# Optimization experiments

Measured on AMD Instinct MI355X. Metric: run time of the kernel, lower is better.

Reference implementation:

```python
import jax, jax.numpy as jnp
import numpy as np

B, H, W, C = 16, 64, 64, 256
WIN, SHIFT, HEADS, NSTYLE, HID = 8, 4, 8, 512, 1024
HB = HEADS // 2   # heads per attention branch
CB = C // 2       # channels per branch
N = WIN * WIN     # tokens per window
EPS = 1e-5


def _rel_index(w):
    coords = np.stack(np.meshgrid(np.arange(w), np.arange(w), indexing='ij'))  # [2,w,w]
    cf = coords.reshape(2, -1)
    rel = (cf[:, :, None] - cf[:, None, :]).transpose(1, 2, 0)  # [N,N,2]
    rel[:, :, 0] += w - 1
    rel[:, :, 1] += w - 1
    rel[:, :, 0] *= 2 * w - 1
    return rel.sum(-1)  # [N,N]


def _sw_mask(Hh, Ww, w, shift):
    img = np.zeros((Hh, Ww))
    cnt = 0
    for hs in (slice(0, -w), slice(-w, -shift), slice(-shift, None)):
        for ws in (slice(0, -w), slice(-w, -shift), slice(-shift, None)):
            img[hs, ws] = cnt
            cnt += 1
    win = img.reshape(Hh // w, w, Ww // w, w).transpose(0, 2, 1, 3).reshape(-1, w * w)
    m = win[:, None, :] - win[:, :, None]
    return np.where(m != 0, -100.0, 0.0).astype(np.float32)  # [nW,N,N]


REL_IDX = _rel_index(WIN)
SW_MASK = jnp.asarray(_sw_mask(H, W, WIN, SHIFT))


def window_partition(x):
    # x: [B,H,W,c] -> [B*nW, N, c]
    b, hh, ww, c = x.shape
    x = x.reshape(b, hh // WIN, WIN, ww // WIN, WIN, c).transpose(0, 1, 3, 2, 4, 5)
    return x.reshape(-1, N, c)


def window_reverse(win):
    c = win.shape[-1]
    x = win.reshape(B, H // WIN, W // WIN, WIN, WIN, c).transpose(0, 1, 3, 2, 4, 5)
    return x.reshape(B, H, W, c)


def _adain(x, style, Wa, ba):
    # x: [B,L,C]; instance norm over L per channel, then style affine
    s = style @ Wa + ba                      # [B, 2C]
    mu_s, std_s = jnp.split(s, 2, axis=1)    # each [B,C]
    mu = x.mean(axis=1, keepdims=True)
    var = ((x - mu) ** 2).mean(axis=1, keepdims=True)
    xn = (x - mu) * jax.lax.rsqrt(var + EPS)
    return mu_s[:, None, :] + std_s[:, None, :] * xn


def _win_attn(q, k, v, rpb, mask):
    # q,k,v: [B_, N, CB]; rpb: [(2w-1)^2, HB]; mask: [nW,N,N] or None
    B_ = q.shape[0]
    d = CB // HB
    q = q.reshape(B_, N, HB, d).transpose(0, 2, 1, 3) * (d ** -0.5)
    k = k.reshape(B_, N, HB, d).transpose(0, 2, 1, 3)
    v = v.reshape(B_, N, HB, d).transpose(0, 2, 1, 3)
    attn = jnp.einsum('bhnd,bhmd->bhnm', q, k)
    bias = rpb[REL_IDX.reshape(-1)].reshape(N, N, HB).transpose(2, 0, 1)
    attn = attn + bias[None]
    if mask is not None:
        nW = mask.shape[0]
        attn = attn.reshape(B_ // nW, nW, HB, N, N) + mask[None, :, None]
        attn = attn.reshape(B_, HB, N, N)
    attn = jax.nn.softmax(attn, axis=-1)
    out = jnp.einsum('bhnm,bhmd->bhnd', attn, v)
    return out.transpose(0, 2, 1, 3).reshape(B_, N, CB)


def setup_inputs() -> dict:
    key = jax.random.key(0)
    ks = jax.random.split(key, 20)
    f = jnp.float32
    return {
        'x': jax.random.normal(ks[0], (B, H * W, C), f),
        'style': jax.random.normal(ks[1], (B, NSTYLE), f),
        'w_qkv': jax.random.normal(ks[2], (C, 3 * C), f) * 0.02,
        'b_qkv': jnp.zeros((3 * C,), f),
        'w_proj': jax.random.normal(ks[3], (C, C), f) * 0.02,
        'b_proj': jnp.zeros((C,), f),
        'w_ada1': jax.random.normal(ks[4], (NSTYLE, 2 * C), f) * 0.02,
        'b_ada1': jnp.concatenate([jnp.zeros((C,), f), jnp.ones((C,), f)]),
        'w_ada2': jax.random.normal(ks[5], (NSTYLE, 2 * C), f) * 0.02,
        'b_ada2': jnp.concatenate([jnp.zeros((C,), f), jnp.ones((C,), f)]),
        'rpb1': jax.random.normal(ks[6], ((2 * WIN - 1) ** 2, HB), f) * 0.02,
        'rpb2': jax.random.normal(ks[7], ((2 * WIN - 1) ** 2, HB), f) * 0.02,
        'w_fc1': jax.random.normal(ks[8], (C, HID), f) * 0.02,
        'b_fc1': jnp.zeros((HID,), f),
        'w_fc2': jax.random.normal(ks[9], (HID, C), f) * 0.02,
        'b_fc2': jnp.zeros((C,), f),
    }


def reference(x, style, w_qkv, b_qkv, w_proj, b_proj, w_ada1, b_ada1,
              w_ada2, b_ada2, rpb1, rpb2, w_fc1, b_fc1, w_fc2, b_fc2):
    Bn, L, Cc = x.shape
    # AdaIN 1
    h = _adain(x, style, w_ada1, b_ada1)                      # [B,L,C]
    qkv = (h @ w_qkv + b_qkv).reshape(Bn, H, W, 3, Cc)
    q, k, v = qkv[..., 0, :], qkv[..., 1, :], qkv[..., 2, :]  # [B,H,W,C]
    # split channels across the two branches
    q1, k1, v1 = q[..., :CB], k[..., :CB], v[..., :CB]
    q2, k2, v2 = q[..., CB:], k[..., CB:], v[..., CB:]
    shift = lambda t: jnp.roll(t, (-SHIFT, -SHIFT), axis=(1, 2))
    # W-MSA branch
    x_w = _win_attn(window_partition(q1), window_partition(k1),
                    window_partition(v1), rpb1, None)
    # SW-MSA branch (shifted windows + mask)
    x_sw = _win_attn(window_partition(shift(q2)), window_partition(shift(k2)),
                     window_partition(shift(v2)), rpb2, SW_MASK)
    xw = window_reverse(x_w)                                  # [B,H,W,CB]
    xsw = jnp.roll(window_reverse(x_sw), (SHIFT, SHIFT), axis=(1, 2))
    attn_out = jnp.concatenate([xw, xsw], axis=-1).reshape(Bn, L, Cc)
    x = x + attn_out @ w_proj + b_proj
    # AdaIN 2 + MLP (exact GELU, as nn.GELU default)
    h2 = _adain(x, style, w_ada2, b_ada2)
    h2 = jax.nn.gelu(h2 @ w_fc1 + b_fc1, approximate=False)
    return x + (h2 @ w_fc2 + b_fc2)
```

## Files before the change

### kernel.cpp

```cpp
#include <hip/hip_runtime.h>
#include <hip/hip_bf16.h>

typedef __bf16 bf16;
typedef __bf16 bf16x4v __attribute__((ext_vector_type(4)));
typedef __bf16 bf16x8v __attribute__((ext_vector_type(8)));
typedef float f32x4 __attribute__((ext_vector_type(4)));
typedef short s16x4 __attribute__((ext_vector_type(4)));

#define DEVINL static __device__ __forceinline__

DEVINL f32x4 mfma16(bf16x8v a, bf16x8v b, f32x4 c) {
  return __builtin_amdgcn_mfma_f32_16x16x32_bf16(a, b, c, 0, 0, 0);
}

DEVINL f32x4 mfma16x16(bf16x4v a, bf16x4v b, f32x4 c) {
#if __has_builtin(__builtin_amdgcn_mfma_f32_16x16x16bf16_1k)
  return __builtin_amdgcn_mfma_f32_16x16x16bf16_1k(
      __builtin_bit_cast(s16x4, a), __builtin_bit_cast(s16x4, b), c, 0, 0, 0);
#else
  f32x4 d;
  asm("v_mfma_f32_16x16x16_bf16 %0, %1, %2, %3"
      : "=v"(d) : "v"(a), "v"(b), "v"(c));
  return d;
#endif
}

__global__ __launch_bounds__(256) void k_style(
    const float* __restrict__ style,
    const float* __restrict__ wa1, const float* __restrict__ ba1,
    const float* __restrict__ wa2, const float* __restrict__ ba2,
    float* __restrict__ s1, float* __restrict__ s2) {
  int bid = blockIdx.x;
  int ng = bid & 31, b = (bid >> 5) & 15, which = bid >> 9;
  int tid = threadIdx.x;
  int nl = tid & 15, kg = tid >> 4;
  int n = ng * 16 + nl;
  const float* wa = which ? wa2 : wa1;
  const float* ba = which ? ba2 : ba1;
  const float* srow = style + b * 512;
  float acc = 0.f;
  #pragma unroll 8
  for (int kk = 0; kk < 32; ++kk) {
    int k = kg + kk * 16;
    acc += srow[k] * wa[k * 512 + n];
  }
  acc += __shfl_xor(acc, 16);
  acc += __shfl_xor(acc, 32);
  __shared__ float red[4][16];
  int l = tid & 63, w = tid >> 6;
  if (l < 16) red[w][nl] = acc;
  __syncthreads();
  if (tid < 16) {
    float S = red[0][tid] + red[1][tid] + red[2][tid] + red[3][tid]
            + ba[ng * 16 + tid];
    (which ? s2 : s1)[b * 512 + ng * 16 + tid] = S;
  }
}

template<int F32>
__global__ __launch_bounds__(256) void k_stats_part(
    const void* __restrict__ xv, float* __restrict__ psum,
    float* __restrict__ psq) {
  int rc = blockIdx.x, b = blockIdx.y;
  int c = threadIdx.x;
  size_t base = (size_t)b * 4096 * 256 + (size_t)rc * 256 * 256 + c;
  float sm = 0.f, q = 0.f;
  #pragma unroll 4
  for (int r = 0; r < 256; ++r) {
    float f;
    if constexpr (F32) f = ((const float*)xv)[base + (size_t)r * 256];
    else               f = (float)((const bf16*)xv)[base + (size_t)r * 256];
    sm += f; q += f * f;
  }
  int o = (b * 16 + rc) * 256 + c;
  psum[o] = sm; psq[o] = q;
}

__global__ __launch_bounds__(256) void k_stats_fin(
    const float* __restrict__ psum, const float* __restrict__ psq,
    const float* __restrict__ s,
    float* __restrict__ scale, float* __restrict__ shift) {
  int b = blockIdx.x, c = threadIdx.x;
  float S = 0.f, Q = 0.f;
  #pragma unroll
  for (int rc = 0; rc < 16; ++rc) {
    S += psum[(b * 16 + rc) * 256 + c];
    Q += psq[(b * 16 + rc) * 256 + c];
  }
  float mean = S * (1.0f/4096.0f);
  float var  = Q * (1.0f/4096.0f) - mean * mean;
  float inv  = rsqrtf(var + 1e-5f);
  float mu_s  = s[b * 512 + c];
  float std_s = s[b * 512 + 256 + c];
  float sc = std_s * inv;
  scale[b * 256 + c] = sc;
  shift[b * 256 + c] = mu_s - sc * mean;
}

template<int F32>
__global__ __launch_bounds__(256) void k_adain(
    const void* __restrict__ in, const float* __restrict__ scale,
    const float* __restrict__ shift, bf16* __restrict__ out) {
  int idx = blockIdx.x * 256 + threadIdx.x;
  int c8 = idx & 31, row = idx >> 5;
  int b = row >> 12, c = c8 * 8;
  const float* scp = &scale[b * 256 + c];
  const float* shp = &shift[b * 256 + c];
  f32x4 sc0 = *(const f32x4*)scp, sc1 = *(const f32x4*)(scp + 4);
  f32x4 sh0 = *(const f32x4*)shp, sh1 = *(const f32x4*)(shp + 4);
  size_t ofs = (size_t)row * 256 + c;
  float f[8];
  if constexpr (F32) {
    f32x4 v0 = *(const f32x4*)&((const float*)in)[ofs];
    f32x4 v1 = *(const f32x4*)&((const float*)in)[ofs + 4];
    f[0]=v0[0]; f[1]=v0[1]; f[2]=v0[2]; f[3]=v0[3];
    f[4]=v1[0]; f[5]=v1[1]; f[6]=v1[2]; f[7]=v1[3];
  } else {
    bf16x8v v = *(const bf16x8v*)&((const bf16*)in)[ofs];
    #pragma unroll
    for (int u = 0; u < 8; ++u) f[u] = (float)v[u];
  }
  bf16x8v o;
  o[0]=(bf16)(sh0[0]+sc0[0]*f[0]); o[1]=(bf16)(sh0[1]+sc0[1]*f[1]);
  o[2]=(bf16)(sh0[2]+sc0[2]*f[2]); o[3]=(bf16)(sh0[3]+sc0[3]*f[3]);
  o[4]=(bf16)(sh1[0]+sc1[0]*f[4]); o[5]=(bf16)(sh1[1]+sc1[1]*f[5]);
  o[6]=(bf16)(sh1[2]+sc1[2]*f[6]); o[7]=(bf16)(sh1[3]+sc1[3]*f[7]);
  *(bf16x8v*)&out[ofs] = o;
}

__global__ __launch_bounds__(256) void k_tr(
    const float* __restrict__ in, bf16* __restrict__ out, int K, int N) {
  __shared__ float t[32][33];
  int bx = blockIdx.x * 32, by = blockIdx.y * 32;
  int tx = threadIdx.x & 31, ty = threadIdx.x >> 5;
  #pragma unroll
  for (int r = 0; r < 32; r += 8)
    t[ty + r][tx] = in[(size_t)(by + ty + r) * N + bx + tx];
  __syncthreads();
  #pragma unroll
  for (int r = 0; r < 32; r += 8)
    out[(size_t)(bx + ty + r) * K + by + tx] = (bf16)t[tx][ty + r];
}

template<int RESMODE, int GELU, int OUTF32>
__global__ __launch_bounds__(512) void k_gemm(
    const bf16* __restrict__ A, const bf16* __restrict__ Bt,
    const float* __restrict__ bias, const void* __restrict__ resv,
    void* __restrict__ outv, int N, int K, int gx) {
  __shared__ bf16 a_sw[256 * 64];
  __shared__ bf16 b_sw[128 * 64];
  int tid = threadIdx.x;
  int l = tid & 63, w = tid >> 6;
  int wr = w >> 1, wc = w & 1;
  int lm = l & 15, lg = l >> 4;

  int nwg = gridDim.x;
  int lin = blockIdx.x;
  int swz = (lin & 7) * (nwg >> 3) + (lin >> 3);
  int bx = swz % gx, by = swz / gx;
  int m0 = by * 256, n0 = bx * 128;

  f32x4 acc[4][4];
  #pragma unroll
  for (int mi = 0; mi < 4; ++mi)
    #pragma unroll
    for (int ni = 0; ni < 4; ++ni)
      acc[mi][ni] = (f32x4){0.f, 0.f, 0.f, 0.f};

  for (int k0 = 0; k0 < K; k0 += 64) {
    #pragma unroll
    for (int i = 0; i < 4; ++i) {
      int slot = i * 512 + tid;
      int r = slot >> 3, cs = slot & 7;
      int c = cs ^ (r & 7);
      const bf16* g = A + (size_t)(m0 + r) * K + k0 + c * 8;
      __builtin_amdgcn_global_load_lds(
          (const __attribute__((address_space(1))) void*)g,
          (__attribute__((address_space(3))) void*)(a_sw + (i * 512 + w * 64) * 8),
          16, 0, 0);
    }
    #pragma unroll
    for (int i = 0; i < 2; ++i) {
      int slot = i * 512 + tid;
      int r = slot >> 3, cs = slot & 7;
      int c = cs ^ (r & 7);
      const bf16* g = Bt + (size_t)(n0 + r) * K + k0 + c * 8;
      __builtin_amdgcn_global_load_lds(
          (const __attribute__((address_space(1))) void*)g,
          (__attribute__((address_space(3))) void*)(b_sw + (i * 512 + w * 64) * 8),
          16, 0, 0);
    }
    __syncthreads();
    #pragma unroll
    for (int kk = 0; kk < 2; ++kk) {
      bf16x8v af[4], bv[4];
      #pragma unroll
      for (int mi = 0; mi < 4; ++mi) {
        int row = wr * 64 + mi * 16 + lm;
        af[mi] = *(const bf16x8v*)&a_sw[row * 64 + (((kk * 4 + lg) ^ (row & 7)) * 8)];
      }
      #pragma unroll
      for (int ni = 0; ni < 4; ++ni) {
        int row = wc * 64 + ni * 16 + lm;
        bv[ni] = *(const bf16x8v*)&b_sw[row * 64 + (((kk * 4 + lg) ^ (row & 7)) * 8)];
      }
      #pragma unroll
      for (int mi = 0; mi < 4; ++mi)
        #pragma unroll
        for (int ni = 0; ni < 4; ++ni)
          acc[mi][ni] = mfma16(af[mi], bv[ni], acc[mi][ni]);
    }
    __syncthreads();
  }
  #pragma unroll
  for (int mi = 0; mi < 4; ++mi) {
    #pragma unroll
    for (int ni = 0; ni < 4; ++ni) {
      int row = m0 + wr * 64 + mi * 16 + lg * 4;
      int col = n0 + wc * 64 + ni * 16 + lm;
      float bv_ = bias[col];
      #pragma unroll
      for (int j = 0; j < 4; ++j) {
        float o = acc[mi][ni][j] + bv_;
        if constexpr (RESMODE == 1)
          o += ((const float*)resv)[(size_t)(row + j) * N + col];
        if constexpr (RESMODE == 2)
          o += (float)((const bf16*)resv)[(size_t)(row + j) * N + col];
        if constexpr (GELU) {
          float z = 1.5957691216057308f * (o + 0.044715f * o * o * o);
          o = o / (1.0f + __expf(-z));
        }
        if constexpr (OUTF32)
          ((float*)outv)[(size_t)(row + j) * N + col] = o;
        else
          ((bf16*)outv)[(size_t)(row + j) * N + col] = (bf16)o;
      }
    }
  }
}

__global__ __launch_bounds__(256) void k_attn(
    const bf16* __restrict__ qkv,
    const float* __restrict__ rpb1, const float* __restrict__ rpb2,
    bf16* __restrict__ aout) {
  __shared__ bf16 vt[128 * 72];
  __shared__ float rl[960];

  int tid = threadIdx.x;
  int bx = blockIdx.x;
  int br = bx & 1, widx = (bx >> 1) & 63, b = bx >> 7;
  int wy = widx >> 3, wx = widx & 7;

  const float* rpb = br ? rpb2 : rpb1;
  #pragma unroll
  for (int t = tid; t < 960; t += 256) {
    int h0 = t / 240, r0 = t - h0 * 240, dy = r0 >> 4, dx = r0 & 15;
    rl[t] = (dx < 15) ? rpb[(dy * 15 + dx) * 4 + h0] : 0.f;
  }

  auto grow = [&](int tok) -> int {
    int y = wy * 8 + (tok >> 3), xc = wx * 8 + (tok & 7);
    if (br) { y = (y + 4) & 63; xc = (xc + 4) & 63; }
    return b * 4096 + y * 64 + xc;
  };

  #pragma unroll
  for (int it = 0; it < 4; ++it) {
    int task = it * 256 + tid;
    int tok = task & 63, chunk = task >> 6;
    bf16x8v v = *(const bf16x8v*)&qkv[(size_t)grow(tok) * 768 + 512 + br * 128 + chunk * 8];
    #pragma unroll
    for (int u = 0; u < 8; ++u) vt[(chunk * 8 + u) * 72 + tok] = v[u];
  }

  int l = tid & 63, h = tid >> 6;
  int lm = l & 15, lg = l >> 4;

  bf16x8v kb[4], qa[4];
  #pragma unroll
  for (int i = 0; i < 4; ++i) {
    size_t rb = (size_t)grow(i * 16 + lm) * 768 + br * 128 + h * 32 + lg * 8;
    qa[i] = *(const bf16x8v*)&qkv[rb];
    kb[i] = *(const bf16x8v*)&qkv[rb + 256];
  }
  __syncthreads();

  bf16x4v vb[2][4];
  #pragma unroll
  for (int ni = 0; ni < 2; ++ni)
    #pragma unroll
    for (int ki = 0; ki < 4; ++ki)
      vb[ni][ki] = *(const bf16x4v*)&vt[(h * 32 + ni * 16 + lm) * 72 + ki * 16 + lg * 4];

  bool need_mask = br && (wy == 7 || wx == 7);

  int ekA[16], idkA[16];
  #pragma unroll
  for (int ki = 0; ki < 4; ++ki)
    #pragma unroll
    for (int j = 0; j < 4; ++j) {
      int ik = ki * 16 + lg * 4 + j;
      ekA[ki * 4 + j] = ik + (ik >> 3) * 8;
      int yk = wy * 8 + (ik >> 3), xk = wx * 8 + (ik & 7);
      idkA[ki * 4 + j] = (yk < 56 ? 0 : (yk < 60 ? 1 : 2)) * 3
                       + (xk < 56 ? 0 : (xk < 60 ? 1 : 2));
    }

  #pragma unroll
  for (int qi = 0; qi < 4; ++qi) {
    f32x4 s[4];
    #pragma unroll
    for (int ki = 0; ki < 4; ++ki)
      s[ki] = mfma16(kb[ki], qa[qi], (f32x4){0.f,0.f,0.f,0.f});

    int iq = qi * 16 + lm;
    int eq = iq + (iq >> 3) * 8;
    int yq = wy * 8 + (iq >> 3), xq = wx * 8 + (iq & 7);
    int idq = (yq < 56 ? 0 : (yq < 60 ? 1 : 2)) * 3
            + (xq < 56 ? 0 : (xq < 60 ? 1 : 2));
    const float* fb = &rl[h * 240 + 119 + eq];

    #pragma unroll
    for (int ki = 0; ki < 4; ++ki)
      #pragma unroll
      for (int j = 0; j < 4; ++j) {
        float val = s[ki][j] * 0.17677669529663687f + fb[-ekA[ki * 4 + j]];
        if (need_mask && idq != idkA[ki * 4 + j]) val -= 100.0f;
        s[ki][j] = val;
      }

    float mx = s[0][0];
    #pragma unroll
    for (int ki = 0; ki < 4; ++ki)
      #pragma unroll
      for (int j = 0; j < 4; ++j) mx = fmaxf(mx, s[ki][j]);
    mx = fmaxf(mx, __shfl_xor(mx, 16));
    mx = fmaxf(mx, __shfl_xor(mx, 32));
    float sum = 0.f;
    #pragma unroll
    for (int ki = 0; ki < 4; ++ki)
      #pragma unroll
      for (int j = 0; j < 4; ++j) {
        float e = __expf(s[ki][j] - mx);
        s[ki][j] = e;
        sum += e;
      }
    sum += __shfl_xor(sum, 16);
    sum += __shfl_xor(sum, 32);
    float rs = 1.0f / sum;

    bf16x4v pa[4];
    #pragma unroll
    for (int ki = 0; ki < 4; ++ki)
      #pragma unroll
      for (int j = 0; j < 4; ++j)
        pa[ki][j] = (bf16)(s[ki][j] * rs);

    f32x4 o[2] = {(f32x4){0.f,0.f,0.f,0.f}, (f32x4){0.f,0.f,0.f,0.f}};
    #pragma unroll
    for (int ki = 0; ki < 4; ++ki) {
      o[0] = mfma16x16(pa[ki], vb[0][ki], o[0]);
      o[1] = mfma16x16(pa[ki], vb[1][ki], o[1]);
    }

    #pragma unroll
    for (int ni = 0; ni < 2; ++ni)
      #pragma unroll
      for (int j = 0; j < 4; ++j) {
        int tok = qi * 16 + lg * 4 + j;
        int col = br * 128 + h * 32 + ni * 16 + lm;
        aout[(size_t)grow(tok) * 256 + col] = (bf16)o[ni][j];
      }
  }
}

extern "C" void kernel_launch(void* const* d_in, const int* in_sizes, int n_in,
                              void* d_out, int out_size, void* d_ws, size_t ws_size,
                              hipStream_t stream) {
  (void)in_sizes; (void)n_in; (void)out_size; (void)ws_size;
  const float* x      = (const float*)d_in[0];
  const float* style  = (const float*)d_in[1];
  const float* w_qkv  = (const float*)d_in[2];
  const float* b_qkv  = (const float*)d_in[3];
  const float* w_proj = (const float*)d_in[4];
  const float* b_proj = (const float*)d_in[5];
  const float* w_ada1 = (const float*)d_in[6];
  const float* b_ada1 = (const float*)d_in[7];
  const float* w_ada2 = (const float*)d_in[8];
  const float* b_ada2 = (const float*)d_in[9];
  const float* rpb1   = (const float*)d_in[10];
  const float* rpb2   = (const float*)d_in[11];
  const float* w_fc1  = (const float*)d_in[12];
  const float* b_fc1  = (const float*)d_in[13];
  const float* w_fc2  = (const float*)d_in[14];
  const float* b_fc2  = (const float*)d_in[15];

  char* ws = (char*)d_ws;
  float* s1     = (float*)(ws + 0);
  float* s2     = (float*)(ws + 32768);
  float* scale1 = (float*)(ws + 65536);
  float* shift1 = (float*)(ws + 81920);
  float* scale2 = (float*)(ws + 98304);
  float* shift2 = (float*)(ws + 114688);
  bf16* wtqkv   = (bf16*)(ws + 131072);
  bf16* wtproj  = (bf16*)(ws + 524288);
  bf16* wtfc1   = (bf16*)(ws + 655360);
  bf16* wtfc2   = (bf16*)(ws + 1179648);
  float* psum   = (float*)(ws + 1703936);
  float* psq    = (float*)(ws + 1966080);
  const size_t BIG = 2228224;
  bf16* xn   = (bf16*)(ws + BIG);
  bf16* qkv  = (bf16*)(ws + BIG + 33554432);
  bf16* attn = (bf16*)(ws + BIG + 134217728);
  bf16* x1   = (bf16*)(ws + BIG + 33554432);
  bf16* xn2  = xn;
  bf16* g    = (bf16*)(ws + BIG + 67108864);

  k_tr<<<dim3(24, 8),  256, 0, stream>>>(w_qkv,  wtqkv,  256, 768);
  k_tr<<<dim3(8, 8),   256, 0, stream>>>(w_proj, wtproj, 256, 256);
  k_tr<<<dim3(32, 8),  256, 0, stream>>>(w_fc1,  wtfc1,  256, 1024);
  k_tr<<<dim3(8, 32),  256, 0, stream>>>(w_fc2,  wtfc2,  1024, 256);

  k_style<<<1024, 256, 0, stream>>>(style, w_ada1, b_ada1, w_ada2, b_ada2, s1, s2);
  k_stats_part<1><<<dim3(16, 16), 256, 0, stream>>>(x, psum, psq);
  k_stats_fin<<<16, 256, 0, stream>>>(psum, psq, s1, scale1, shift1);
  k_adain<1><<<8192, 256, 0, stream>>>(x, scale1, shift1, xn);

  k_gemm<0,0,0><<<1536, 512, 0, stream>>>(
      xn, wtqkv, b_qkv, nullptr, qkv, 768, 256, 6);

  k_attn<<<2048, 256, 0, stream>>>(qkv, rpb1, rpb2, attn);

  k_gemm<1,0,0><<<512, 512, 0, stream>>>(
      attn, wtproj, b_proj, x, x1, 256, 256, 2);

  k_stats_part<0><<<dim3(16, 16), 256, 0, stream>>>(x1, psum, psq);
  k_stats_fin<<<16, 256, 0, stream>>>(psum, psq, s2, scale2, shift2);
  k_adain<0><<<8192, 256, 0, stream>>>(x1, scale2, shift2, xn2);

  for (int ch = 0; ch < 2; ++ch) {
    size_t ro = (size_t)ch * 32768;
    k_gemm<0,1,0><<<1024, 512, 0, stream>>>(
        xn2 + ro * 256, wtfc1, b_fc1, nullptr, g, 1024, 256, 8);
    k_gemm<2,0,1><<<256, 512, 0, stream>>>(
        g, wtfc2, b_fc2, x1 + ro * 256,
        (float*)d_out + ro * 256, 256, 1024, 2);
  }
}
```

Before: 334.5 us.

## Add 128x128 GEMM variant for narrow-N GEMMs and swizzle attention V transpose

Adds a 4-wave GEMM kernel with 128x128 tiles and uses it for the proj and fc2 GEMMs (N=256). This doubles the workgroup count so more CUs are occupied on these narrow outputs, at the cost of less reuse of the A tile per block. Separately, the attention V transpose store into LDS now uses token-major task mapping with an XOR swizzle on the column, read back with the matching swizzle, to reduce LDS bank conflicts.

```diff
diff --git a/kernel.cpp b/kernel.cpp
--- a/kernel.cpp
+++ b/kernel.cpp
@@ -8,6 +8,8 @@
 typedef short s16x4 __attribute__((ext_vector_type(4)));
 
 #define DEVINL static __device__ __forceinline__
+#define AS1 __attribute__((address_space(1)))
+#define AS3 __attribute__((address_space(3)))
 
 DEVINL f32x4 mfma16(bf16x8v a, bf16x8v b, f32x4 c) {
   return __builtin_amdgcn_mfma_f32_16x16x32_bf16(a, b, c, 0, 0, 0);
@@ -175,8 +177,7 @@
       int c = cs ^ (r & 7);
       const bf16* g = A + (size_t)(m0 + r) * K + k0 + c * 8;
       __builtin_amdgcn_global_load_lds(
-          (const __attribute__((address_space(1))) void*)g,
-          (__attribute__((address_space(3))) void*)(a_sw + (i * 512 + w * 64) * 8),
+          (const AS1 void*)g, (AS3 void*)(a_sw + (i * 512 + w * 64) * 8),
           16, 0, 0);
     }
     #pragma unroll
@@ -186,8 +187,7 @@
       int c = cs ^ (r & 7);
       const bf16* g = Bt + (size_t)(n0 + r) * K + k0 + c * 8;
       __builtin_amdgcn_global_load_lds(
-          (const __attribute__((address_space(1))) void*)g,
-          (__attribute__((address_space(3))) void*)(b_sw + (i * 512 + w * 64) * 8),
+          (const AS1 void*)g, (AS3 void*)(b_sw + (i * 512 + w * 64) * 8),
           16, 0, 0);
     }
     __syncthreads();
@@ -239,6 +239,99 @@
   }
 }
 
+template<int RESMODE, int GELU, int OUTF32>
+__global__ __launch_bounds__(256) void k_gemm4(
+    const bf16* __restrict__ A, const bf16* __restrict__ Bt,
+    const float* __restrict__ bias, const void* __restrict__ resv,
+    void* __restrict__ outv, int N, int K, int gx) {
+  __shared__ bf16 a_sw[128 * 64];
+  __shared__ bf16 b_sw[128 * 64];
+  int tid = threadIdx.x;
+  int l = tid & 63, w = tid >> 6;
+  int wr = w >> 1, wc = w & 1;
+  int lm = l & 15, lg = l >> 4;
+
+  int nwg = gridDim.x;
+  int lin = blockIdx.x;
+  int swz = (lin & 7) * (nwg >> 3) + (lin >> 3);
+  int bx = swz % gx, by = swz / gx;
+  int m0 = by * 128, n0 = bx * 128;
+
+  f32x4 acc[4][4];
+  #pragma unroll
+  for (int mi = 0; mi < 4; ++mi)
+    #pragma unroll
+    for (int ni = 0; ni < 4; ++ni)
+      acc[mi][ni] = (f32x4){0.f, 0.f, 0.f, 0.f};
+
+  for (int k0 = 0; k0 < K; k0 += 64) {
+    #pragma unroll
+    for (int i = 0; i < 4; ++i) {
+      int slot = i * 256 + tid;
+      int r = slot >> 3, cs = slot & 7;
+      int c = cs ^ (r & 7);
+      __builtin_amdgcn_global_load_lds(
+          (const AS1 void*)(A + (size_t)(m0 + r) * K + k0 + c * 8),
+          (AS3 void*)(a_sw + (i * 256 + w * 64) * 8), 16, 0, 0);
+    }
+    #pragma unroll
+    for (int i = 0; i < 4; ++i) {
+      int slot = i * 256 + tid;
+      int r = slot >> 3, cs = slot & 7;
+      int c = cs ^ (r & 7);
+      __builtin_amdgcn_global_load_lds(
+          (const AS1 void*)(Bt + (size_t)(n0 + r) * K + k0 + c * 8),
+          (AS3 void*)(b_sw + (i * 256 + w * 64) * 8), 16, 0, 0);
+    }
+    __syncthreads();
+    #pragma unroll
+    for (int kk = 0; kk < 2; ++kk) {
+      bf16x8v af[4], bv[4];
+      #pragma unroll
+      for (int mi = 0; mi < 4; ++mi) {
+        int row = wr * 64 + mi * 16 + lm;
+        af[mi] = *(const bf16x8v*)&a_sw[row * 64 + (((kk * 4 + lg) ^ (row & 7)) * 8)];
+      }
+      #pragma unroll
+      for (int ni = 0; ni < 4; ++ni) {
+        int row = wc * 64 + ni * 16 + lm;
+        bv[ni] = *(const bf16x8v*)&b_sw[row * 64 + (((kk * 4 + lg) ^ (row & 7)) * 8)];
+      }
+      #pragma unroll
+      for (int mi = 0; mi < 4; ++mi)
+        #pragma unroll
+        for (int ni = 0; ni < 4; ++ni)
+          acc[mi][ni] = mfma16(af[mi], bv[ni], acc[mi][ni]);
+    }
+    __syncthreads();
+  }
+  #pragma unroll
+  for (int mi = 0; mi < 4; ++mi) {
+    #pragma unroll
+    for (int ni = 0; ni < 4; ++ni) {
+      int row = m0 + wr * 64 + mi * 16 + lg * 4;
+      int col = n0 + wc * 64 + ni * 16 + lm;
+      float bv_ = bias[col];
+      #pragma unroll
+      for (int j = 0; j < 4; ++j) {
+        float o = acc[mi][ni][j] + bv_;
+        if constexpr (RESMODE == 1)
+          o += ((const float*)resv)[(size_t)(row + j) * N + col];
+        if constexpr (RESMODE == 2)
+          o += (float)((const bf16*)resv)[(size_t)(row + j) * N + col];
+        if constexpr (GELU) {
+          float z = 1.5957691216057308f * (o + 0.044715f * o * o * o);
+          o = o / (1.0f + __expf(-z));
+        }
+        if constexpr (OUTF32)
+          ((float*)outv)[(size_t)(row + j) * N + col] = o;
+        else
+          ((bf16*)outv)[(size_t)(row + j) * N + col] = (bf16)o;
+      }
+    }
+  }
+}
+
 __global__ __launch_bounds__(256) void k_attn(
     const bf16* __restrict__ qkv,
     const float* __restrict__ rpb1, const float* __restrict__ rpb2,
@@ -267,10 +360,11 @@
   #pragma unroll
   for (int it = 0; it < 4; ++it) {
     int task = it * 256 + tid;
-    int tok = task & 63, chunk = task >> 6;
+    int tok = task >> 4, chunk = task & 15;
     bf16x8v v = *(const bf16x8v*)&qkv[(size_t)grow(tok) * 768 + 512 + br * 128 + chunk * 8];
-    #pragma unroll
-    for (int u = 0; u < 8; ++u) vt[(chunk * 8 + u) * 72 + tok] = v[u];
+    int tsw = tok ^ ((chunk & 7) << 3);
+    #pragma unroll
+    for (int u = 0; u < 8; ++u) vt[(chunk * 8 + u) * 72 + tsw] = v[u];
   }
 
   int l = tid & 63, h = tid >> 6;
@@ -289,8 +383,11 @@
   #pragma unroll
   for (int ni = 0; ni < 2; ++ni)
     #pragma unroll
-    for (int ki = 0; ki < 4; ++ki)
-      vb[ni][ki] = *(const bf16x4v*)&vt[(h * 32 + ni * 16 + lm) * 72 + ki * 16 + lg * 4];
+    for (int ki = 0; ki < 4; ++ki) {
+      int row = h * 32 + ni * 16 + lm;
+      int col = (ki * 16 + lg * 4) ^ (((row >> 3) & 7) << 3);
+      vb[ni][ki] = *(const bf16x4v*)&vt[row * 72 + col];
+    }
 
   bool need_mask = br && (wy == 7 || wx == 7);
 
@@ -431,7 +528,7 @@
 
   k_attn<<<2048, 256, 0, stream>>>(qkv, rpb1, rpb2, attn);
 
-  k_gemm<1,0,0><<<512, 512, 0, stream>>>(
+  k_gemm4<1,0,0><<<1024, 256, 0, stream>>>(
       attn, wtproj, b_proj, x, x1, 256, 256, 2);
 
   k_stats_part<0><<<dim3(16, 16), 256, 0, stream>>>(x1, psum, psq);
@@ -442,7 +539,7 @@
     size_t ro = (size_t)ch * 32768;
     k_gemm<0,1,0><<<1024, 512, 0, stream>>>(
         xn2 + ro * 256, wtfc1, b_fc1, nullptr, g, 1024, 256, 8);
-    k_gemm<2,0,1><<<256, 512, 0, stream>>>(
+    k_gemm4<2,0,1><<<512, 256, 0, stream>>>(
         g, wtfc2, b_fc2, x1 + ro * 256,
         (float*)d_out + ro * 256, 256, 1024, 2);
   }
```

After: 326.3 us. -2.5%, faster.
